# Optimization experiments

Hardware: AMD Instinct MI355X
Metric: run time of the kernel (lower is better)

## Reference

```python
import jax, jax.numpy as jnp
from jax import lax
import numpy as np

K = 4            # prototypes per class: 3 kmeans centroids + 1 backbone
EPS = 0.1        # sinkhorn entropic regularization
MAX_ITER = 100
THRESH = 0.01
KM_ITERS = 10    # Lloyd iterations (replaces host-side sklearn KMeans)
HW = 28          # the original reshapes pred to 28x28, fixing n = 784


def setup_inputs():
    key = jax.random.key(0)
    k1, k2, k3, k4 = jax.random.split(key, 4)
    b, n, d, c = 32, HW * HW, 1024, 20
    return {
        "query": jax.random.normal(k1, (b, n, d), dtype=jnp.float32),
        "score": jax.random.uniform(k2, (b, n, c), dtype=jnp.float32),
        "label": jax.random.randint(k3, (b, c), 0, 2),
        "gt": jax.random.randint(k4, (b, HW, HW), 0, c + 1),
        "weights": jnp.array([1.0, 1.0, 0.0, -1.0], dtype=jnp.float32),
    }


def _assign(dq, cen, selfm):
    # dq [b,m,d], cen [b,c,j,d], selfm [b,c,m] float mask -> one-hot labels, counts
    x2 = jnp.sum(dq * dq, axis=-1)                                   # [b,m]
    d2 = (x2[:, None, :, None]
          - 2.0 * jnp.einsum('bmd,bcjd->bcmj', dq, cen)
          + jnp.sum(cen * cen, axis=-1)[:, :, None, :])              # [b,c,m,j]
    oh = jax.nn.one_hot(jnp.argmin(d2, axis=-1), cen.shape[2], dtype=dq.dtype) * selfm[..., None]
    return oh, oh.sum(axis=2)


def _sinkhorn(Km, u, v):
    # vectorized over the [b,c] pair grid, per-pair early exit as in the torch loop
    def cond(st):
        it, r, cc, done = st
        return (it < MAX_ITER) & jnp.logical_not(jnp.all(done))

    def body(st):
        it, r, cc, done = st
        r1 = u / jnp.einsum('bcnj,bcj->bcn', Km, cc)
        c1 = v / jnp.einsum('bcnj,bcn->bcj', Km, r1)
        err = jnp.mean(jnp.abs(r1 - r), axis=-1)                     # [b,c]
        r = jnp.where(done[..., None], r, r1)
        cc = jnp.where(done[..., None], cc, c1)
        done = done | (err < THRESH)
        return it + 1, r, cc, done

    st = (jnp.int32(0), jnp.ones_like(u), jnp.ones_like(v),
          jnp.zeros(Km.shape[:2], dtype=bool))
    _, r, cc, _ = lax.while_loop(cond, body, st)
    return r[..., :, None] * cc[..., None, :] * Km                   # [b,c,n,K]


def _forward(query, score, label, gt, weights):
    b, n, d = query.shape
    c = score.shape[2]
    dq, ds = query[:, ::2, :], score[:, ::2, :]                      # stride-2 downsample
    m = dq.shape[1]
    cls_assign = jnp.argmax(ds, axis=-1)                             # [b,m]
    sel = cls_assign[:, None, :] == jnp.arange(c)[None, :, None]     # [b,c,m]
    selfm = sel.astype(query.dtype)
    cnt = selfm.sum(-1)                                              # [b,c]
    valid = (label > 0) & (cnt >= K)

    # ---- masked Lloyd's k-means with k-1 = 3 clusters per (image, class) pair
    order = jnp.argsort((~sel).astype(jnp.int32), axis=-1)           # masked points first
    init_idx = order[..., :K - 1]                                    # [b,c,3]
    cen = dq[jnp.arange(b)[:, None, None], init_idx]                 # [b,c,3,d]

    def km_step(cen, _):
        oh, kcnt = _assign(dq, cen, selfm)
        sums = jnp.einsum('bmd,bcmj->bcjd', dq, oh)
        cen = jnp.where(kcnt[..., None] > 0,
                        sums / jnp.maximum(kcnt, 1.0)[..., None], cen)
        return cen, None

    cen, _ = lax.scan(km_step, cen, None, length=KM_ITERS)
    oh, kcnt = _assign(dq, cen, selfm)                               # final labels

    # ---- sort centroids by mean cluster score (descending)
    sm = ds.mean(axis=-1)                                            # [b,m]
    avg = jnp.where(kcnt > 0,
                    jnp.einsum('bm,bcmj->bcj', sm, oh) / jnp.maximum(kcnt, 1.0),
                    -jnp.inf)
    ordj = jnp.argsort(-avg, axis=-1)                                # [b,c,3]
    cen = jnp.take_along_axis(cen, ordj[..., None], axis=2)

    # ---- backbone prototype = mean over unselected downsampled tokens
    un = 1.0 - selfm
    backbone = jnp.einsum('bmd,bcm->bcd', dq, un) / jnp.maximum(m - cnt, 1.0)[..., None]
    protos = jnp.concatenate([cen, backbone[:, :, None, :]], axis=2)  # [b,c,4,d]

    # ---- OT between query[0] tokens and the 4 prototypes (original uses query[0] always)
    q0 = query[0]
    q0h = q0 / jnp.maximum(jnp.linalg.norm(q0, axis=-1, keepdims=True), 1e-12)
    ph = protos / jnp.maximum(jnp.linalg.norm(protos, axis=-1, keepdims=True), 1e-12)
    sim = jnp.einsum('nd,bcjd->bcnj', q0h, ph)                       # [b,c,n,4]
    Km = lax.stop_gradient(jnp.exp(-(1.0 - sim) / EPS))              # torch.no_grad
    u = jnp.full((b, c, n), 1.0 / n, dtype=query.dtype)
    v = jnp.full((b, c, K), 1.0 / K, dtype=query.dtype)
    T = lax.stop_gradient(_sinkhorn(Km, u, v))                       # [b,c,n,4]

    valid = valid & jnp.logical_not(jnp.any(jnp.isnan(T), axis=(2, 3)))
    pred = jnp.einsum('bcnj,j->bcn', T, weights)                     # [b,c,n]

    # ---- BCE vs gt masks (28x28 -> 28x28 bilinear resize is the identity)
    y = (gt.reshape(b, -1)[:, None, :] == (jnp.arange(c) + 1)[None, :, None]).astype(pred.dtype)
    p = jnp.clip(pred, 0.0, 1.0)
    bce = -(y * jnp.maximum(jnp.log(p), -100.0)
            + (1.0 - y) * jnp.maximum(jnp.log(1.0 - p), -100.0)).mean(axis=-1)  # [b,c]
    bce = jnp.where(valid, bce, 0.0)
    total_n = valid.sum().astype(pred.dtype)
    return bce.sum() / (total_n + 1e-4)


def reference(query, score, label, gt, weights):
    return _forward(query, score, label, gt, weights)
```

## Files before the change

kernel.cpp:

```cpp
#include <hip/hip_runtime.h>
#include <cmath>

#define BB 32
#define NN 784
#define MM 392
#define DD 1024
#define CC 20
#define JJ 3
#define KP 4
#define KM_ITERS 10
#define GMAX 64
#define NCOL (BB * CC * KP)

typedef __attribute__((ext_vector_type(8))) short bf16x8;
typedef __attribute__((ext_vector_type(4))) float f32x4;

__device__ inline unsigned short f2bf(float x) {
  unsigned int u = __float_as_uint(x);
  u += 0x7FFFu + ((u >> 16) & 1u);
  return (unsigned short)(u >> 16);
}
__device__ inline float bf2f(unsigned short h) {
  return __uint_as_float(((unsigned int)h) << 16);
}
__device__ inline void f2bf2(float x, unsigned short& hi, unsigned short& lo) {
  hi = f2bf(x);
  lo = f2bf(x - bf2f(hi));
}
__device__ inline void store_bf4(unsigned short* baseh, unsigned short* basel,
                                 int idx4, float4 v) {
  ushort4 h, l;
  f2bf2(v.x, h.x, l.x); f2bf2(v.y, h.y, l.y);
  f2bf2(v.z, h.z, l.z); f2bf2(v.w, h.w, l.w);
  ((ushort4*)baseh)[idx4] = h;
  ((ushort4*)basel)[idx4] = l;
}

__global__ void k_cls(const float* __restrict__ score, int* __restrict__ cls,
                      float* __restrict__ sm, int* __restrict__ cnt) {
  int t = blockIdx.x * blockDim.x + threadIdx.x;
  if (t >= BB * MM) return;
  int b = t / MM, i = t - b * MM;
  const float* s = score + ((size_t)b * NN + 2 * i) * CC;
  float best = s[0]; int bi = 0; float acc = s[0];
  #pragma unroll
  for (int c = 1; c < CC; c++) { float v = s[c]; acc += v; if (v > best) { best = v; bi = c; } }
  cls[t] = bi;
  sm[t] = acc / (float)CC;
  atomicAdd(&cnt[b * CC + bi], 1);
}

__global__ void k_valid(const int* __restrict__ label, const int* __restrict__ cnt,
                        int* __restrict__ vlist, int* __restrict__ cpos, int* __restrict__ nvp) {
  __shared__ int sf[1024];
  int t = threadIdx.x;
  int flag = 0;
  if (t < BB * CC) flag = (label[t] > 0 && cnt[t] >= KP) ? 1 : 0;
  sf[t] = flag;
  __syncthreads();
  for (int off = 1; off < 1024; off <<= 1) {
    int v = sf[t];
    int add = (t >= off) ? sf[t - off] : 0;
    __syncthreads();
    sf[t] = v + add;
    __syncthreads();
  }
  if (t < BB * CC) {
    int pos = sf[t] - flag;
    cpos[t] = flag ? pos : -1;
    if (flag) vlist[pos] = t;
  }
  if (t == 0) *nvp = sf[BB * CC - 1];
}

__global__ __launch_bounds__(256) void k_csum(const float* __restrict__ query,
    const int* __restrict__ cls, float* __restrict__ classsum) {
  int b = blockIdx.x, ch = blockIdx.y;
  int tid = threadIdx.x, lane = tid & 63, wv = tid >> 6;
  __shared__ float acc[4][CC][64];
  __shared__ int s_cls[MM];
  #pragma unroll
  for (int c = 0; c < CC; c++) acc[wv][c][lane] = 0.f;
  for (int i = tid; i < MM; i += 256) s_cls[i] = cls[b * MM + i];
  __syncthreads();
  const float* qb = query + (size_t)b * NN * DD + ch * 64 + lane;
  int i0 = wv * 98;
  #pragma unroll 4
  for (int r = 0; r < 98; r++) {
    int i = i0 + r;
    float v = qb[(size_t)(2 * i) * DD];
    int cl = s_cls[i];
    acc[wv][cl][lane] += v;
  }
  __syncthreads();
  for (int cc = wv; cc < CC; cc += 4) {
    float s = acc[0][cc][lane] + acc[1][cc][lane] + acc[2][cc][lane] + acc[3][cc][lane];
    classsum[((size_t)(b * CC + cc)) * DD + ch * 64 + lane] = s;
  }
}

__global__ __launch_bounds__(512) void k_gram(
    const float* __restrict__ query, const int* __restrict__ cls,
    const int* __restrict__ cpos, const float* __restrict__ sm,
    unsigned short* __restrict__ phh, unsigned short* __restrict__ phl) {
  int bc = blockIdx.x;
  if (cpos[bc] < 0) return;
  int b = bc / CC, c = bc - b * CC;
  int tid = threadIdx.x, lane = tid & 63, wv = tid >> 6;
  const float* qb = query + (size_t)b * NN * DD;
  __shared__ int s_wtot[8];
  __shared__ int s_list[GMAX];
  __shared__ __align__(16) float Xs[GMAX][132];
  __shared__ float Gl[GMAX][65];
  __shared__ float s_w[JJ][GMAX];
  __shared__ int s_rank[JJ];
  __shared__ float s_red2[6];

  int flag = 0;
  if (tid < MM) flag = (cls[b * MM + tid] == c) ? 1 : 0;
  unsigned long long msk = __ballot(flag);
  int wp = __popcll(msk & ((1ull << lane) - 1ull));
  if (lane == 0) s_wtot[wv] = __popcll(msk);
  __syncthreads();
  int off = 0, mtot = 0;
  #pragma unroll
  for (int w = 0; w < 8; w++) { int t = s_wtot[w]; if (w < wv) off += t; mtot += t; }
  int mc = mtot > GMAX ? GMAX : mtot;
  if (flag) { int pos = off + wp; if (pos < GMAX) s_list[pos] = tid; }
  __syncthreads();

  const float* pb[4] = {nullptr, nullptr, nullptr, nullptr};
  float* xd[4] = {nullptr, nullptr, nullptr, nullptr};
  #pragma unroll
  for (int s = 0; s < 4; s++) {
    int e = tid + s * 512;
    if (e < mc * 32) {
      pb[s] = qb + (size_t)(2 * s_list[e >> 5]) * DD + (e & 31) * 4;
      xd[s] = &Xs[e >> 5][(e & 31) * 4];
    }
  }

  int T = (mc + 1) >> 1;
  int ntile = T * (T + 1) / 2;
  int ti_[2], tj_[2];
  float a00[2], a01[2], a10[2], a11[2];
  #pragma unroll
  for (int s = 0; s < 2; s++) {
    ti_[s] = -1; tj_[s] = 0;
    a00[s] = 0.f; a01[s] = 0.f; a10[s] = 0.f; a11[s] = 0.f;
    int p = tid + s * 512;
    if (p < ntile) {
      int i = (int)floorf((sqrtf(8.0f * (float)p + 1.0f) - 1.0f) * 0.5f);
      while ((i + 1) * (i + 2) / 2 <= p) i++;
      while (i * (i + 1) / 2 > p) i--;
      ti_[s] = i; tj_[s] = p - i * (i + 1) / 2;
    }
  }

  float4 cur[4], nxt[4];
  #pragma unroll
  for (int s = 0; s < 4; s++) {
    cur[s] = make_float4(0.f, 0.f, 0.f, 0.f);
    nxt[s] = make_float4(0.f, 0.f, 0.f, 0.f);
    if (pb[s]) cur[s] = *(const float4*)(pb[s]);
  }
  for (int ch = 0; ch < 8; ch++) {
    __syncthreads();
    #pragma unroll
    for (int s = 0; s < 4; s++) if (pb[s]) *(float4*)xd[s] = cur[s];
    if (ch < 7) {
      #pragma unroll
      for (int s = 0; s < 4; s++) if (pb[s]) nxt[s] = *(const float4*)(pb[s] + (ch + 1) * 128);
    }
    __syncthreads();
    #pragma unroll
    for (int s = 0; s < 2; s++) {
      if (ti_[s] >= 0) {
        const float4* xr0 = (const float4*)&Xs[2 * ti_[s]][0];
        const float4* xr1 = (const float4*)&Xs[2 * ti_[s] + 1][0];
        const float4* xc0 = (const float4*)&Xs[2 * tj_[s]][0];
        const float4* xc1 = (const float4*)&Xs[2 * tj_[s] + 1][0];
        float s00 = 0.f, s01 = 0.f, s10 = 0.f, s11 = 0.f;
        #pragma unroll
        for (int kk = 0; kk < 32; kk++) {
          float4 u0 = xr0[kk], u1 = xr1[kk], w0 = xc0[kk], w1 = xc1[kk];
          s00 += u0.x * w0.x + u0.y * w0.y + u0.z * w0.z + u0.w * w0.w;
          s01 += u0.x * w1.x + u0.y * w1.y + u0.z * w1.z + u0.w * w1.w;
          s10 += u1.x * w0.x + u1.y * w0.y + u1.z * w0.z + u1.w * w0.w;
          s11 += u1.x * w1.x + u1.y * w1.y + u1.z * w1.z + u1.w * w1.w;
        }
        a00[s] += s00; a01[s] += s01; a10[s] += s10; a11[s] += s11;
      }
    }
    #pragma unroll
    for (int s = 0; s < 4; s++) cur[s] = nxt[s];
  }

  #pragma unroll
  for (int s = 0; s < 2; s++) {
    if (ti_[s] >= 0) {
      int r0 = 2 * ti_[s], r1 = r0 + 1, c0 = 2 * tj_[s], c1 = c0 + 1;
      if (r0 < mc && c0 < mc) { Gl[r0][c0] = a00[s]; Gl[c0][r0] = a00[s]; }
      if (r0 < mc && c1 < mc) { Gl[r0][c1] = a01[s]; Gl[c1][r0] = a01[s]; }
      if (r1 < mc && c0 < mc) { Gl[r1][c0] = a10[s]; Gl[c0][r1] = a10[s]; }
      if (r1 < mc && c1 < mc) { Gl[r1][c1] = a11[s]; Gl[c1][r1] = a11[s]; }
    }
  }
  __syncthreads();

  if (wv == 0) {
    bool act = lane < mc;
    float smv = act ? sm[b * MM + s_list[lane]] : 0.f;
    s_w[0][lane] = (lane == 0) ? 1.f : 0.f;
    s_w[1][lane] = (lane == 1) ? 1.f : 0.f;
    s_w[2][lane] = (lane == 2) ? 1.f : 0.f;
    int aj = 0, n0 = 0, n1 = 0, n2 = 0;
    for (int it = 0; it <= KM_ITERS; it++) {
      float h0 = 0.f, h1 = 0.f, h2 = 0.f;
      if (act) {
        for (int i = 0; i < mc; i++) {
          float g = Gl[lane][i];
          h0 += s_w[0][i] * g; h1 += s_w[1][i] * g; h2 += s_w[2][i] * g;
        }
      }
      float t0 = s_w[0][lane] * h0, t1 = s_w[1][lane] * h1, t2 = s_w[2][lane] * h2;
      for (int o = 1; o < 64; o <<= 1) {
        t0 += __shfl_xor(t0, o, 64); t1 += __shfl_xor(t1, o, 64); t2 += __shfl_xor(t2, o, 64);
      }
      float e0 = t0 - 2.f * h0, e1 = t1 - 2.f * h1, e2 = t2 - 2.f * h2;
      aj = 0; float bv = e0;
      if (e1 < bv) { bv = e1; aj = 1; }
      if (e2 < bv) { bv = e2; aj = 2; }
      n0 = __popcll(__ballot(act && aj == 0));
      n1 = __popcll(__ballot(act && aj == 1));
      n2 = __popcll(__ballot(act && aj == 2));
      if (it == KM_ITERS) break;
      if (act) {
        if (n0 > 0) s_w[0][lane] = (aj == 0) ? 1.f / (float)n0 : 0.f;
        if (n1 > 0) s_w[1][lane] = (aj == 1) ? 1.f / (float)n1 : 0.f;
        if (n2 > 0) s_w[2][lane] = (aj == 2) ? 1.f / (float)n2 : 0.f;
      }
    }
    float s0 = (act && aj == 0) ? smv : 0.f;
    float s1 = (act && aj == 1) ? smv : 0.f;
    float s2 = (act && aj == 2) ? smv : 0.f;
    for (int o = 1; o < 64; o <<= 1) {
      s0 += __shfl_xor(s0, o, 64); s1 += __shfl_xor(s1, o, 64); s2 += __shfl_xor(s2, o, 64);
    }
    if (lane == 0) {
      float avg[JJ];
      avg[0] = (n0 > 0) ? s0 / (float)n0 : -INFINITY;
      avg[1] = (n1 > 0) ? s1 / (float)n1 : -INFINITY;
      avg[2] = (n2 > 0) ? s2 / (float)n2 : -INFINITY;
      bool used[JJ] = {false, false, false};
      for (int s = 0; s < JJ; s++) {
        int bi = -1; float bv = 0.f;
        for (int j = 0; j < JJ; j++)
          if (!used[j] && (bi < 0 || avg[j] > bv)) { bi = j; bv = avg[j]; }
        used[bi] = true; s_rank[bi] = s;
      }
    }
  }
  __syncthreads();

  float4 a0 = make_float4(0.f, 0.f, 0.f, 0.f), a1 = make_float4(0.f, 0.f, 0.f, 0.f);
  int j = tid >> 7, q = tid & 127;
  if (tid < 384) {
    for (int g = 0; g < mc; g++) {
      float w = s_w[j][g];
      if (w != 0.f) {
        const float4* row = (const float4*)(qb + (size_t)(2 * s_list[g]) * DD);
        float4 v0 = row[q], v1 = row[q + 128];
        a0.x += w * v0.x; a0.y += w * v0.y; a0.z += w * v0.z; a0.w += w * v0.w;
        a1.x += w * v1.x; a1.y += w * v1.y; a1.z += w * v1.z; a1.w += w * v1.w;
      }
    }
    float ssq = a0.x * a0.x + a0.y * a0.y + a0.z * a0.z + a0.w * a0.w
              + a1.x * a1.x + a1.y * a1.y + a1.z * a1.z + a1.w * a1.w;
    #pragma unroll
    for (int o = 1; o < 64; o <<= 1) ssq += __shfl_xor(ssq, o, 64);
    if (lane == 0) s_red2[wv] = ssq;
  }
  __syncthreads();
  if (tid < 384) {
    float nrm = fmaxf(sqrtf(s_red2[2 * j] + s_red2[2 * j + 1]), 1e-12f);
    size_t rowoff = ((size_t)bc * KP + s_rank[j]) * DD;
    float4 o0 = make_float4(a0.x / nrm, a0.y / nrm, a0.z / nrm, a0.w / nrm);
    float4 o1 = make_float4(a1.x / nrm, a1.y / nrm, a1.z / nrm, a1.w / nrm);
    store_bf4(phh + rowoff, phl + rowoff, q, o0);
    store_bf4(phh + rowoff, phl + rowoff, q + 128, o1);
  }
}

__global__ __launch_bounds__(256) void k_backbone(const float* __restrict__ classsum,
    const int* __restrict__ cpos, const int* __restrict__ cnt,
    unsigned short* __restrict__ phh, unsigned short* __restrict__ phl) {
  int bc = blockIdx.x;
  if (cpos[bc] < 0) return;
  int b = bc / CC;
  int tid = threadIdx.x, lane = tid & 63, wv = tid >> 6;
  __shared__ float s_red[4];
  __shared__ float s_nrm;
  float4 ts = make_float4(0.f, 0.f, 0.f, 0.f);
  for (int c2 = 0; c2 < CC; c2++) {
    float4 v = *(const float4*)(classsum + ((size_t)(b * CC + c2)) * DD + tid * 4);
    ts.x += v.x; ts.y += v.y; ts.z += v.z; ts.w += v.w;
  }
  float4 cs = *(const float4*)(classsum + (size_t)bc * DD + tid * 4);
  float denom = fmaxf((float)(MM - cnt[bc]), 1.f);
  float4 v = make_float4((ts.x - cs.x) / denom, (ts.y - cs.y) / denom,
                         (ts.z - cs.z) / denom, (ts.w - cs.w) / denom);
  float pp = v.x * v.x + v.y * v.y + v.z * v.z + v.w * v.w;
  for (int o = 1; o < 64; o <<= 1) pp += __shfl_xor(pp, o, 64);
  if (lane == 0) s_red[wv] = pp;
  __syncthreads();
  if (tid == 0) s_nrm = fmaxf(sqrtf(s_red[0] + s_red[1] + s_red[2] + s_red[3]), 1e-12f);
  __syncthreads();
  float nrm = s_nrm;
  size_t rowoff = ((size_t)bc * KP + 3) * DD;
  store_bf4(phh + rowoff, phl + rowoff, tid,
            make_float4(v.x / nrm, v.y / nrm, v.z / nrm, v.w / nrm));
}

__global__ void k_q0h(const float* __restrict__ query,
                      unsigned short* __restrict__ q0hh, unsigned short* __restrict__ q0hl) {
  int n = blockIdx.x;
  const float* src = query + (size_t)n * DD;
  float ss = 0.f;
  for (int k = threadIdx.x; k < DD; k += 64) { float v = src[k]; ss += v * v; }
  for (int o = 32; o > 0; o >>= 1) ss += __shfl_xor(ss, o, 64);
  float nrm = fmaxf(sqrtf(ss), 1e-12f);
  for (int k = threadIdx.x; k < DD; k += 64) {
    unsigned short hi, lo;
    f2bf2(src[k] / nrm, hi, lo);
    q0hh[(size_t)n * DD + k] = hi;
    q0hl[(size_t)n * DD + k] = lo;
  }
}

__global__ __launch_bounds__(64) void k_gemm(
    const unsigned short* __restrict__ Ah, const unsigned short* __restrict__ Al,
    const unsigned short* __restrict__ Bh, const unsigned short* __restrict__ Bl,
    const int* __restrict__ vlist, const int* __restrict__ nvp,
    float* __restrict__ P) {
  int nv4 = 4 * *nvp;
  int n0 = blockIdx.y * 64;
  if (n0 >= nv4) return;
  int m0 = blockIdx.x * 64;
  int lane = threadIdx.x;
  int kh = lane >> 4;
  int lr = lane & 15;

  const unsigned short* pa_h[4]; const unsigned short* pa_l[4];
  #pragma unroll
  for (int mi = 0; mi < 4; mi++) {
    size_t o = (size_t)(m0 + mi * 16 + lr) * DD + kh * 8;
    pa_h[mi] = Ah + o; pa_l[mi] = Al + o;
  }
  const unsigned short* pb_h[4]; const unsigned short* pb_l[4];
  #pragma unroll
  for (int ni = 0; ni < 4; ni++) {
    int col = n0 + ni * 16 + lr;
    int cc = (col < nv4) ? col : 0;
    size_t o = ((size_t)vlist[cc >> 2] * KP + (cc & 3)) * DD + kh * 8;
    pb_h[ni] = Bh + o; pb_l[ni] = Bl + o;
  }

  f32x4 acc[4][4];
  #pragma unroll
  for (int mi = 0; mi < 4; mi++)
    #pragma unroll
    for (int ni = 0; ni < 4; ni++) acc[mi][ni] = (f32x4){0.f, 0.f, 0.f, 0.f};

  for (int k0 = 0; k0 < DD; k0 += 32) {
    bf16x8 ah[4], al[4], bh[4], bl[4];
    #pragma unroll
    for (int i = 0; i < 4; i++) {
      ah[i] = *(const bf16x8*)(pa_h[i] + k0);
      al[i] = *(const bf16x8*)(pa_l[i] + k0);
      bh[i] = *(const bf16x8*)(pb_h[i] + k0);
      bl[i] = *(const bf16x8*)(pb_l[i] + k0);
    }
    #pragma unroll
    for (int mi = 0; mi < 4; mi++)
      #pragma unroll
      for (int ni = 0; ni < 4; ni++) {
        acc[mi][ni] = __builtin_amdgcn_mfma_f32_16x16x32_bf16(ah[mi], bh[ni], acc[mi][ni], 0, 0, 0);
        acc[mi][ni] = __builtin_amdgcn_mfma_f32_16x16x32_bf16(ah[mi], bl[ni], acc[mi][ni], 0, 0, 0);
        acc[mi][ni] = __builtin_amdgcn_mfma_f32_16x16x32_bf16(al[mi], bh[ni], acc[mi][ni], 0, 0, 0);
      }
  }

  #pragma unroll
  for (int ni = 0; ni < 4; ni++) {
    int col = n0 + ni * 16 + lr;
    #pragma unroll
    for (int mi = 0; mi < 4; mi++) {
      int m = m0 + mi * 16 + kh * 4;
      if (m < NN) {
        *(f32x4*)(P + (size_t)col * NN + m) = acc[mi][ni];
      }
    }
  }
}

__global__ __launch_bounds__(256) void k_sink(const float* __restrict__ P,
    const int* __restrict__ cpos, const int* __restrict__ gt,
    const float* __restrict__ wts, float* __restrict__ bce, int* __restrict__ vld) {
  int bc = blockIdx.x; int b = bc / CC, c = bc - b * CC;
  int tid = threadIdx.x;
  if (cpos[bc] < 0) {
    if (tid == 0) { bce[bc] = 0.f; vld[bc] = 0; }
    return;
  }
  int p = cpos[bc];
  int lane = tid & 63, wv = tid >> 6;
  __shared__ float ccv[KP];
  __shared__ float wred[4][5];
  __shared__ float s_err;
  __shared__ int s_nan;
  float4 kv[4]; float rr[4];
  #pragma unroll
  for (int s4 = 0; s4 < 4; s4++) {
    int n = tid + 256 * s4;
    kv[s4] = make_float4(0.f, 0.f, 0.f, 0.f); rr[s4] = 1.f;
    if (n < NN) {
      float v[KP];
      #pragma unroll
      for (int q = 0; q < KP; q++)
        v[q] = P[((size_t)(4 * p + q)) * NN + n];
      float4 o;
      o.x = expf(-(1.0f - v[0]) / 0.1f);
      o.y = expf(-(1.0f - v[1]) / 0.1f);
      o.z = expf(-(1.0f - v[2]) / 0.1f);
      o.w = expf(-(1.0f - v[3]) / 0.1f);
      kv[s4] = o;
    }
  }
  if (tid < KP) ccv[tid] = 1.f;
  if (tid == 0) s_nan = 0;
  __syncthreads();
  const float uu = 1.0f / (float)NN, vv = 1.0f / (float)KP;
  for (int it = 0; it < 100; it++) {
    float c0 = ccv[0], c1 = ccv[1], c2 = ccv[2], c3 = ccv[3];
    float dsum = 0.f, p0 = 0.f, p1 = 0.f, p2 = 0.f, p3 = 0.f;
    #pragma unroll
    for (int s4 = 0; s4 < 4; s4++) {
      int n = tid + 256 * s4;
      if (n < NN) {
        float4 k4 = kv[s4];
        float S = k4.x * c0 + k4.y * c1 + k4.z * c2 + k4.w * c3;
        float r1 = uu / S;
        dsum += fabsf(r1 - rr[s4]);
        rr[s4] = r1;
        p0 += k4.x * r1; p1 += k4.y * r1; p2 += k4.z * r1; p3 += k4.w * r1;
      }
    }
    for (int o = 32; o > 0; o >>= 1) {
      dsum += __shfl_down(dsum, o, 64);
      p0 += __shfl_down(p0, o, 64); p1 += __shfl_down(p1, o, 64);
      p2 += __shfl_down(p2, o, 64); p3 += __shfl_down(p3, o, 64);
    }
    if (lane == 0) { wred[wv][0] = dsum; wred[wv][1] = p0; wred[wv][2] = p1; wred[wv][3] = p2; wred[wv][4] = p3; }
    __syncthreads();
    if (tid == 0) {
      float d = 0.f, q0 = 0.f, q1 = 0.f, q2 = 0.f, q3 = 0.f;
      for (int w = 0; w < 4; w++) { d += wred[w][0]; q0 += wred[w][1]; q1 += wred[w][2]; q2 += wred[w][3]; q3 += wred[w][4]; }
      ccv[0] = vv / q0; ccv[1] = vv / q1; ccv[2] = vv / q2; ccv[3] = vv / q3;
      s_err = d / (float)NN;
    }
    __syncthreads();
    if (s_err < 0.01f) break;
  }
  float w0 = wts[0], w1 = wts[1], w2 = wts[2], w3 = wts[3];
  float cc0 = ccv[0], cc1 = ccv[1], cc2 = ccv[2], cc3 = ccv[3];
  float bsum = 0.f; int nanloc = 0;
  const int* gtb = gt + b * NN;
  #pragma unroll
  for (int s4 = 0; s4 < 4; s4++) {
    int n = tid + 256 * s4;
    if (n < NN) {
      float4 k4 = kv[s4];
      float rv = rr[s4];
      float T0 = rv * cc0 * k4.x, T1 = rv * cc1 * k4.y, T2 = rv * cc2 * k4.z, T3 = rv * cc3 * k4.w;
      if (T0 != T0 || T1 != T1 || T2 != T2 || T3 != T3) nanloc = 1;
      float pred = T0 * w0 + T1 * w1 + T2 * w2 + T3 * w3;
      float pcl = fminf(fmaxf(pred, 0.f), 1.f);
      float t = (gtb[n] == c + 1) ? fmaxf(logf(pcl), -100.f) : fmaxf(logf(1.f - pcl), -100.f);
      bsum += t;
    }
  }
  if (nanloc) s_nan = 1;
  for (int o = 32; o > 0; o >>= 1) bsum += __shfl_down(bsum, o, 64);
  if (lane == 0) wred[wv][0] = bsum;
  __syncthreads();
  if (tid == 0) {
    float tot = wred[0][0] + wred[1][0] + wred[2][0] + wred[3][0];
    if (s_nan) { bce[bc] = 0.f; vld[bc] = 0; }
    else { bce[bc] = -(tot / (float)NN); vld[bc] = 1; }
  }
}

__global__ void k_final(const float* __restrict__ bce, const int* __restrict__ vld,
                        float* __restrict__ out) {
  __shared__ float rs[256];
  __shared__ float rc[256];
  float s = 0.f, cv = 0.f;
  for (int t = threadIdx.x; t < BB * CC; t += 256) { s += bce[t]; cv += (float)vld[t]; }
  rs[threadIdx.x] = s; rc[threadIdx.x] = cv; __syncthreads();
  for (int o = 128; o > 0; o >>= 1) {
    if (threadIdx.x < o) { rs[threadIdx.x] += rs[threadIdx.x + o]; rc[threadIdx.x] += rc[threadIdx.x + o]; }
    __syncthreads();
  }
  if (threadIdx.x == 0) out[0] = rs[0] / (rc[0] + 0.0001f);
}

extern "C" void kernel_launch(void* const* d_in, const int* in_sizes, int n_in,
                              void* d_out, int out_size, void* d_ws, size_t ws_size,
                              hipStream_t stream) {
  (void)in_sizes; (void)n_in; (void)out_size; (void)ws_size;
  const float* query = (const float*)d_in[0];
  const float* score = (const float*)d_in[1];
  const int*   label = (const int*)d_in[2];
  const int*   gt    = (const int*)d_in[3];
  const float* wts   = (const float*)d_in[4];
  float* ws = (float*)d_ws;

  size_t off = 0;
  int* cls = (int*)(ws + off);            off += (size_t)BB * MM;
  int* cnt = (int*)(ws + off);            off += (size_t)BB * CC;
  float* sm = ws + off;                   off += (size_t)BB * MM;
  int* vlist = (int*)(ws + off);          off += (size_t)BB * CC;
  int* cpos = (int*)(ws + off);           off += (size_t)BB * CC;
  int* nvp = (int*)(ws + off);            off += 16;
  float* classsum = ws + off;             off += (size_t)BB * CC * DD;
  unsigned short* q0hh = (unsigned short*)(ws + off);  off += (size_t)NN * DD / 2;
  unsigned short* q0hl = (unsigned short*)(ws + off);  off += (size_t)NN * DD / 2;
  unsigned short* phh = (unsigned short*)(ws + off);   off += (size_t)BB * CC * KP * DD / 2;
  unsigned short* phl = (unsigned short*)(ws + off);   off += (size_t)BB * CC * KP * DD / 2;
  float* P = ws + off;                    off += (size_t)NCOL * NN;
  float* bce = ws + off;                  off += (size_t)BB * CC;
  int* vld = (int*)(ws + off);            off += (size_t)BB * CC;

  hipMemsetAsync(cnt, 0, (size_t)BB * CC * sizeof(int), stream);
  k_cls<<<(BB * MM + 255) / 256, 256, 0, stream>>>(score, cls, sm, cnt);
  k_valid<<<1, 1024, 0, stream>>>(label, cnt, vlist, cpos, nvp);
  k_csum<<<dim3(BB, 16), 256, 0, stream>>>(query, cls, classsum);
  k_gram<<<BB * CC, 512, 0, stream>>>(query, cls, cpos, sm, phh, phl);
  k_backbone<<<BB * CC, 256, 0, stream>>>(classsum, cpos, cnt, phh, phl);
  k_q0h<<<NN, 64, 0, stream>>>(query, q0hh, q0hl);
  dim3 gg((NN + 63) / 64, NCOL / 64);
  k_gemm<<<gg, 64, 0, stream>>>(q0hh, q0hl, phh, phl, vlist, nvp, P);
  k_sink<<<BB * CC, 256, 0, stream>>>(P, cpos, gt, wts, bce, vld);
  k_final<<<1, 256, 0, stream>>>(bce, vld, (float*)d_out);
}
```

Baseline: 301.0 us.

## Fuse preprocessing kernels, fold backbone into gram, finalize via atomics in sinkhorn

Merges the class argmax, validity flags, query-row normalization and per-batch total sums into one multi-role k_prep launch. The backbone prototype is now computed inside k_gram from a per-batch total minus the class's own rows, replacing the classsum buffer and the k_backbone kernel. The final reduction moves into k_sink through atomics and a last-block counter, removing k_final and the memset. The GEMM drops valid-column compaction and computes all columns, including invalid pairs whose prototypes are never written, in exchange for fewer launches and no prefix scan.

```diff
diff --git a/kernel.cpp b/kernel.cpp
--- a/kernel.cpp
+++ b/kernel.cpp
@@ -11,6 +11,8 @@
 #define KM_ITERS 10
 #define GMAX 64
 #define NCOL (BB * CC * KP)
+#define NQ0B 98
+#define NTSB (BB * 16)
 
 typedef __attribute__((ext_vector_type(8))) short bf16x8;
 typedef __attribute__((ext_vector_type(4))) float f32x4;
@@ -36,75 +38,86 @@
   ((ushort4*)basel)[idx4] = l;
 }
 
-__global__ void k_cls(const float* __restrict__ score, int* __restrict__ cls,
-                      float* __restrict__ sm, int* __restrict__ cnt) {
-  int t = blockIdx.x * blockDim.x + threadIdx.x;
-  if (t >= BB * MM) return;
-  int b = t / MM, i = t - b * MM;
-  const float* s = score + ((size_t)b * NN + 2 * i) * CC;
-  float best = s[0]; int bi = 0; float acc = s[0];
-  #pragma unroll
-  for (int c = 1; c < CC; c++) { float v = s[c]; acc += v; if (v > best) { best = v; bi = c; } }
-  cls[t] = bi;
-  sm[t] = acc / (float)CC;
-  atomicAdd(&cnt[b * CC + bi], 1);
-}
-
-__global__ void k_valid(const int* __restrict__ label, const int* __restrict__ cnt,
-                        int* __restrict__ vlist, int* __restrict__ cpos, int* __restrict__ nvp) {
-  __shared__ int sf[1024];
-  int t = threadIdx.x;
-  int flag = 0;
-  if (t < BB * CC) flag = (label[t] > 0 && cnt[t] >= KP) ? 1 : 0;
-  sf[t] = flag;
-  __syncthreads();
-  for (int off = 1; off < 1024; off <<= 1) {
-    int v = sf[t];
-    int add = (t >= off) ? sf[t - off] : 0;
-    __syncthreads();
-    sf[t] = v + add;
-    __syncthreads();
-  }
-  if (t < BB * CC) {
-    int pos = sf[t] - flag;
-    cpos[t] = flag ? pos : -1;
-    if (flag) vlist[pos] = t;
-  }
-  if (t == 0) *nvp = sf[BB * CC - 1];
-}
-
-__global__ __launch_bounds__(256) void k_csum(const float* __restrict__ query,
-    const int* __restrict__ cls, float* __restrict__ classsum) {
-  int b = blockIdx.x, ch = blockIdx.y;
+__global__ __launch_bounds__(512) void k_prep(
+    const float* __restrict__ score, const float* __restrict__ query,
+    const int* __restrict__ label,
+    int* __restrict__ cls, float* __restrict__ sm, int* __restrict__ valid,
+    float* __restrict__ totalsum,
+    unsigned short* __restrict__ q0hh, unsigned short* __restrict__ q0hl,
+    float* __restrict__ gred) {
+  int blk = blockIdx.x;
   int tid = threadIdx.x, lane = tid & 63, wv = tid >> 6;
-  __shared__ float acc[4][CC][64];
-  __shared__ int s_cls[MM];
-  #pragma unroll
-  for (int c = 0; c < CC; c++) acc[wv][c][lane] = 0.f;
-  for (int i = tid; i < MM; i += 256) s_cls[i] = cls[b * MM + i];
-  __syncthreads();
-  const float* qb = query + (size_t)b * NN * DD + ch * 64 + lane;
-  int i0 = wv * 98;
-  #pragma unroll 4
-  for (int r = 0; r < 98; r++) {
-    int i = i0 + r;
-    float v = qb[(size_t)(2 * i) * DD];
-    int cl = s_cls[i];
-    acc[wv][cl][lane] += v;
-  }
-  __syncthreads();
-  for (int cc = wv; cc < CC; cc += 4) {
-    float s = acc[0][cc][lane] + acc[1][cc][lane] + acc[2][cc][lane] + acc[3][cc][lane];
-    classsum[((size_t)(b * CC + cc)) * DD + ch * 64 + lane] = s;
+  __shared__ int s_cnt[CC];
+  __shared__ float sa[8][64];
+
+  if (blk < BB) {
+    int b = blk;
+    if (tid < CC) s_cnt[tid] = 0;
+    __syncthreads();
+    if (tid < MM) {
+      const float4* s4 = (const float4*)(score + ((size_t)b * NN + 2 * tid) * CC);
+      float4 r[5];
+      #pragma unroll
+      for (int k = 0; k < 5; k++) r[k] = s4[k];
+      const float* s = (const float*)r;
+      float best = s[0]; int bi = 0; float acc = s[0];
+      #pragma unroll
+      for (int c = 1; c < CC; c++) { float v = s[c]; acc += v; if (v > best) { best = v; bi = c; } }
+      cls[b * MM + tid] = bi;
+      sm[b * MM + tid] = acc / (float)CC;
+      atomicAdd(&s_cnt[bi], 1);
+    }
+    __syncthreads();
+    if (tid < CC) {
+      int cv = s_cnt[tid];
+      valid[b * CC + tid] = (label[b * CC + tid] > 0 && cv >= KP) ? 1 : 0;
+    }
+    if (blk == 0 && tid == 0) { gred[0] = 0.f; gred[1] = 0.f; ((int*)gred)[2] = 0; }
+  } else if (blk < BB + NQ0B) {
+    int n = (blk - BB) * 8 + wv;
+    const float* src = query + (size_t)n * DD;
+    float v[16];
+    float ss = 0.f;
+    #pragma unroll
+    for (int j = 0; j < 16; j++) { v[j] = src[lane + 64 * j]; ss += v[j] * v[j]; }
+    #pragma unroll
+    for (int o = 32; o > 0; o >>= 1) ss += __shfl_xor(ss, o, 64);
+    float nrm = fmaxf(sqrtf(ss), 1e-12f);
+    #pragma unroll
+    for (int j = 0; j < 16; j++) {
+      unsigned short hi, lo;
+      f2bf2(v[j] / nrm, hi, lo);
+      q0hh[(size_t)n * DD + lane + 64 * j] = hi;
+      q0hl[(size_t)n * DD + lane + 64 * j] = lo;
+    }
+  } else {
+    int t = blk - BB - NQ0B;
+    int b = t >> 4, ch = t & 15;
+    const float* qb = query + (size_t)b * NN * DD + ch * 64 + lane;
+    float a = 0.f;
+    #pragma unroll 7
+    for (int r = 0; r < 49; r++) {
+      int i = wv * 49 + r;
+      a += qb[(size_t)(2 * i) * DD];
+    }
+    sa[wv][lane] = a;
+    __syncthreads();
+    if (wv == 0) {
+      float s = 0.f;
+      #pragma unroll
+      for (int w = 0; w < 8; w++) s += sa[w][lane];
+      totalsum[(size_t)b * DD + ch * 64 + lane] = s;
+    }
   }
 }
 
 __global__ __launch_bounds__(512) void k_gram(
     const float* __restrict__ query, const int* __restrict__ cls,
-    const int* __restrict__ cpos, const float* __restrict__ sm,
+    const int* __restrict__ valid, const float* __restrict__ sm,
+    const float* __restrict__ totalsum,
     unsigned short* __restrict__ phh, unsigned short* __restrict__ phl) {
   int bc = blockIdx.x;
-  if (cpos[bc] < 0) return;
+  if (!valid[bc]) return;
   int b = bc / CC, c = bc - b * CC;
   int tid = threadIdx.x, lane = tid & 63, wv = tid >> 6;
   const float* qb = query + (size_t)b * NN * DD;
@@ -114,7 +127,7 @@
   __shared__ float Gl[GMAX][65];
   __shared__ float s_w[JJ][GMAX];
   __shared__ int s_rank[JJ];
-  __shared__ float s_red2[6];
+  __shared__ float s_red2[8];
 
   int flag = 0;
   if (tid < MM) flag = (cls[b * MM + tid] == c) ? 1 : 0;
@@ -265,7 +278,7 @@
 
   float4 a0 = make_float4(0.f, 0.f, 0.f, 0.f), a1 = make_float4(0.f, 0.f, 0.f, 0.f);
   int j = tid >> 7, q = tid & 127;
-  if (tid < 384) {
+  if (j < 3) {
     for (int g = 0; g < mc; g++) {
       float w = s_w[j][g];
       if (w != 0.f) {
@@ -275,77 +288,42 @@
         a1.x += w * v1.x; a1.y += w * v1.y; a1.z += w * v1.z; a1.w += w * v1.w;
       }
     }
-    float ssq = a0.x * a0.x + a0.y * a0.y + a0.z * a0.z + a0.w * a0.w
-              + a1.x * a1.x + a1.y * a1.y + a1.z * a1.z + a1.w * a1.w;
-    #pragma unroll
-    for (int o = 1; o < 64; o <<= 1) ssq += __shfl_xor(ssq, o, 64);
-    if (lane == 0) s_red2[wv] = ssq;
-  }
+  } else {
+    for (int g = 0; g < mc; g++) {
+      const float4* row = (const float4*)(qb + (size_t)(2 * s_list[g]) * DD);
+      float4 v0 = row[q], v1 = row[q + 128];
+      a0.x += v0.x; a0.y += v0.y; a0.z += v0.z; a0.w += v0.w;
+      a1.x += v1.x; a1.y += v1.y; a1.z += v1.z; a1.w += v1.w;
+    }
+    const float4* tb = (const float4*)(totalsum + (size_t)b * DD);
+    float4 t0 = tb[q], t1 = tb[q + 128];
+    float denom = fmaxf((float)(MM - mtot), 1.f);
+    float inv = 1.f / denom;
+    a0.x = (t0.x - a0.x) * inv; a0.y = (t0.y - a0.y) * inv;
+    a0.z = (t0.z - a0.z) * inv; a0.w = (t0.w - a0.w) * inv;
+    a1.x = (t1.x - a1.x) * inv; a1.y = (t1.y - a1.y) * inv;
+    a1.z = (t1.z - a1.z) * inv; a1.w = (t1.w - a1.w) * inv;
+  }
+  float ssq = a0.x * a0.x + a0.y * a0.y + a0.z * a0.z + a0.w * a0.w
+            + a1.x * a1.x + a1.y * a1.y + a1.z * a1.z + a1.w * a1.w;
+  #pragma unroll
+  for (int o = 1; o < 64; o <<= 1) ssq += __shfl_xor(ssq, o, 64);
+  if (lane == 0) s_red2[wv] = ssq;
   __syncthreads();
-  if (tid < 384) {
-    float nrm = fmaxf(sqrtf(s_red2[2 * j] + s_red2[2 * j + 1]), 1e-12f);
-    size_t rowoff = ((size_t)bc * KP + s_rank[j]) * DD;
-    float4 o0 = make_float4(a0.x / nrm, a0.y / nrm, a0.z / nrm, a0.w / nrm);
-    float4 o1 = make_float4(a1.x / nrm, a1.y / nrm, a1.z / nrm, a1.w / nrm);
-    store_bf4(phh + rowoff, phl + rowoff, q, o0);
-    store_bf4(phh + rowoff, phl + rowoff, q + 128, o1);
-  }
-}
-
-__global__ __launch_bounds__(256) void k_backbone(const float* __restrict__ classsum,
-    const int* __restrict__ cpos, const int* __restrict__ cnt,
-    unsigned short* __restrict__ phh, unsigned short* __restrict__ phl) {
-  int bc = blockIdx.x;
-  if (cpos[bc] < 0) return;
-  int b = bc / CC;
-  int tid = threadIdx.x, lane = tid & 63, wv = tid >> 6;
-  __shared__ float s_red[4];
-  __shared__ float s_nrm;
-  float4 ts = make_float4(0.f, 0.f, 0.f, 0.f);
-  for (int c2 = 0; c2 < CC; c2++) {
-    float4 v = *(const float4*)(classsum + ((size_t)(b * CC + c2)) * DD + tid * 4);
-    ts.x += v.x; ts.y += v.y; ts.z += v.z; ts.w += v.w;
-  }
-  float4 cs = *(const float4*)(classsum + (size_t)bc * DD + tid * 4);
-  float denom = fmaxf((float)(MM - cnt[bc]), 1.f);
-  float4 v = make_float4((ts.x - cs.x) / denom, (ts.y - cs.y) / denom,
-                         (ts.z - cs.z) / denom, (ts.w - cs.w) / denom);
-  float pp = v.x * v.x + v.y * v.y + v.z * v.z + v.w * v.w;
-  for (int o = 1; o < 64; o <<= 1) pp += __shfl_xor(pp, o, 64);
-  if (lane == 0) s_red[wv] = pp;
-  __syncthreads();
-  if (tid == 0) s_nrm = fmaxf(sqrtf(s_red[0] + s_red[1] + s_red[2] + s_red[3]), 1e-12f);
-  __syncthreads();
-  float nrm = s_nrm;
-  size_t rowoff = ((size_t)bc * KP + 3) * DD;
-  store_bf4(phh + rowoff, phl + rowoff, tid,
-            make_float4(v.x / nrm, v.y / nrm, v.z / nrm, v.w / nrm));
-}
-
-__global__ void k_q0h(const float* __restrict__ query,
-                      unsigned short* __restrict__ q0hh, unsigned short* __restrict__ q0hl) {
-  int n = blockIdx.x;
-  const float* src = query + (size_t)n * DD;
-  float ss = 0.f;
-  for (int k = threadIdx.x; k < DD; k += 64) { float v = src[k]; ss += v * v; }
-  for (int o = 32; o > 0; o >>= 1) ss += __shfl_xor(ss, o, 64);
-  float nrm = fmaxf(sqrtf(ss), 1e-12f);
-  for (int k = threadIdx.x; k < DD; k += 64) {
-    unsigned short hi, lo;
-    f2bf2(src[k] / nrm, hi, lo);
-    q0hh[(size_t)n * DD + k] = hi;
-    q0hl[(size_t)n * DD + k] = lo;
-  }
+  float nrm = fmaxf(sqrtf(s_red2[2 * j] + s_red2[2 * j + 1]), 1e-12f);
+  int prow = (j < 3) ? s_rank[j] : 3;
+  size_t rowoff = ((size_t)bc * KP + prow) * DD;
+  float4 o0 = make_float4(a0.x / nrm, a0.y / nrm, a0.z / nrm, a0.w / nrm);
+  float4 o1 = make_float4(a1.x / nrm, a1.y / nrm, a1.z / nrm, a1.w / nrm);
+  store_bf4(phh + rowoff, phl + rowoff, q, o0);
+  store_bf4(phh + rowoff, phl + rowoff, q + 128, o1);
 }
 
 __global__ __launch_bounds__(64) void k_gemm(
     const unsigned short* __restrict__ Ah, const unsigned short* __restrict__ Al,
     const unsigned short* __restrict__ Bh, const unsigned short* __restrict__ Bl,
-    const int* __restrict__ vlist, const int* __restrict__ nvp,
     float* __restrict__ P) {
-  int nv4 = 4 * *nvp;
   int n0 = blockIdx.y * 64;
-  if (n0 >= nv4) return;
   int m0 = blockIdx.x * 64;
   int lane = threadIdx.x;
   int kh = lane >> 4;
@@ -361,8 +339,7 @@
   #pragma unroll
   for (int ni = 0; ni < 4; ni++) {
     int col = n0 + ni * 16 + lr;
-    int cc = (col < nv4) ? col : 0;
-    size_t o = ((size_t)vlist[cc >> 2] * KP + (cc & 3)) * DD + kh * 8;
+    size_t o = (size_t)col * DD + kh * 8;
     pb_h[ni] = Bh + o; pb_l[ni] = Bl + o;
   }
 
@@ -405,114 +382,109 @@
 }
 
 __global__ __launch_bounds__(256) void k_sink(const float* __restrict__ P,
-    const int* __restrict__ cpos, const int* __restrict__ gt,
-    const float* __restrict__ wts, float* __restrict__ bce, int* __restrict__ vld) {
+    const int* __restrict__ valid, const int* __restrict__ gt,
+    const float* __restrict__ wts, float* __restrict__ gred, float* __restrict__ out) {
   int bc = blockIdx.x; int b = bc / CC, c = bc - b * CC;
   int tid = threadIdx.x;
-  if (cpos[bc] < 0) {
-    if (tid == 0) { bce[bc] = 0.f; vld[bc] = 0; }
-    return;
-  }
-  int p = cpos[bc];
   int lane = tid & 63, wv = tid >> 6;
-  __shared__ float ccv[KP];
-  __shared__ float wred[4][5];
-  __shared__ float s_err;
-  __shared__ int s_nan;
-  float4 kv[4]; float rr[4];
-  #pragma unroll
-  for (int s4 = 0; s4 < 4; s4++) {
-    int n = tid + 256 * s4;
-    kv[s4] = make_float4(0.f, 0.f, 0.f, 0.f); rr[s4] = 1.f;
-    if (n < NN) {
-      float v[KP];
+  float bce_out = 0.f; int vld_out = 0;
+
+  if (valid[bc]) {
+    __shared__ float ccv[KP];
+    __shared__ float wred[4][5];
+    __shared__ float s_err;
+    __shared__ int s_nan;
+    float4 kv[4]; float rr[4];
+    #pragma unroll
+    for (int s4 = 0; s4 < 4; s4++) {
+      int n = tid + 256 * s4;
+      kv[s4] = make_float4(0.f, 0.f, 0.f, 0.f); rr[s4] = 1.f;
+      if (n < NN) {
+        float v[KP];
+        #pragma unroll
+        for (int q = 0; q < KP; q++)
+          v[q] = P[((size_t)(4 * bc + q)) * NN + n];
+        float4 o;
+        o.x = expf(-(1.0f - v[0]) / 0.1f);
+        o.y = expf(-(1.0f - v[1]) / 0.1f);
+        o.z = expf(-(1.0f - v[2]) / 0.1f);
+        o.w = expf(-(1.0f - v[3]) / 0.1f);
+        kv[s4] = o;
+      }
+    }
+    if (tid < KP) ccv[tid] = 1.f;
+    if (tid == 0) s_nan = 0;
+    __syncthreads();
+    const float uu = 1.0f / (float)NN, vv = 1.0f / (float)KP;
+    for (int it = 0; it < 100; it++) {
+      float c0 = ccv[0], c1 = ccv[1], c2 = ccv[2], c3 = ccv[3];
+      float dsum = 0.f, p0 = 0.f, p1 = 0.f, p2 = 0.f, p3 = 0.f;
       #pragma unroll
-      for (int q = 0; q < KP; q++)
-        v[q] = P[((size_t)(4 * p + q)) * NN + n];
-      float4 o;
-      o.x = expf(-(1.0f - v[0]) / 0.1f);
-      o.y = expf(-(1.0f - v[1]) / 0.1f);
-      o.z = expf(-(1.0f - v[2]) / 0.1f);
-      o.w = expf(-(1.0f - v[3]) / 0.1f);
-      kv[s4] = o;
-    }
-  }
-  if (tid < KP) ccv[tid] = 1.f;
-  if (tid == 0) s_nan = 0;
-  __syncthreads();
-  const float uu = 1.0f / (float)NN, vv = 1.0f / (float)KP;
-  for (int it = 0; it < 100; it++) {
-    float c0 = ccv[0], c1 = ccv[1], c2 = ccv[2], c3 = ccv[3];
-    float dsum = 0.f, p0 = 0.f, p1 = 0.f, p2 = 0.f, p3 = 0.f;
+      for (int s4 = 0; s4 < 4; s4++) {
+        int n = tid + 256 * s4;
+        if (n < NN) {
+          float4 k4 = kv[s4];
+          float S = k4.x * c0 + k4.y * c1 + k4.z * c2 + k4.w * c3;
+          float r1 = uu / S;
+          dsum += fabsf(r1 - rr[s4]);
+          rr[s4] = r1;
+          p0 += k4.x * r1; p1 += k4.y * r1; p2 += k4.z * r1; p3 += k4.w * r1;
+        }
+      }
+      for (int o = 32; o > 0; o >>= 1) {
+        dsum += __shfl_down(dsum, o, 64);
+        p0 += __shfl_down(p0, o, 64); p1 += __shfl_down(p1, o, 64);
+        p2 += __shfl_down(p2, o, 64); p3 += __shfl_down(p3, o, 64);
+      }
+      if (lane == 0) { wred[wv][0] = dsum; wred[wv][1] = p0; wred[wv][2] = p1; wred[wv][3] = p2; wred[wv][4] = p3; }
+      __syncthreads();
+      if (tid == 0) {
+        float d = 0.f, q0 = 0.f, q1 = 0.f, q2 = 0.f, q3 = 0.f;
+        for (int w = 0; w < 4; w++) { d += wred[w][0]; q0 += wred[w][1]; q1 += wred[w][2]; q2 += wred[w][3]; q3 += wred[w][4]; }
+        ccv[0] = vv / q0; ccv[1] = vv / q1; ccv[2] = vv / q2; ccv[3] = vv / q3;
+        s_err = d / (float)NN;
+      }
+      __syncthreads();
+      if (s_err < 0.01f) break;
+    }
+    float w0 = wts[0], w1 = wts[1], w2 = wts[2], w3 = wts[3];
+    float cc0 = ccv[0], cc1 = ccv[1], cc2 = ccv[2], cc3 = ccv[3];
+    float bsum = 0.f; int nanloc = 0;
+    const int* gtb = gt + b * NN;
     #pragma unroll
     for (int s4 = 0; s4 < 4; s4++) {
       int n = tid + 256 * s4;
       if (n < NN) {
         float4 k4 = kv[s4];
-        float S = k4.x * c0 + k4.y * c1 + k4.z * c2 + k4.w * c3;
-        float r1 = uu / S;
-        dsum += fabsf(r1 - rr[s4]);
-        rr[s4] = r1;
-        p0 += k4.x * r1; p1 += k4.y * r1; p2 += k4.z * r1; p3 += k4.w * r1;
-      }
-    }
-    for (int o = 32; o > 0; o >>= 1) {
-      dsum += __shfl_down(dsum, o, 64);
-      p0 += __shfl_down(p0, o, 64); p1 += __shfl_down(p1, o, 64);
-      p2 += __shfl_down(p2, o, 64); p3 += __shfl_down(p3, o, 64);
-    }
-    if (lane == 0) { wred[wv][0] = dsum; wred[wv][1] = p0; wred[wv][2] = p1; wred[wv][3] = p2; wred[wv][4] = p3; }
+        float rv = rr[s4];
+        float T0 = rv * cc0 * k4.x, T1 = rv * cc1 * k4.y, T2 = rv * cc2 * k4.z, T3 = rv * cc3 * k4.w;
+        if (T0 != T0 || T1 != T1 || T2 != T2 || T3 != T3) nanloc = 1;
+        float pred = T0 * w0 + T1 * w1 + T2 * w2 + T3 * w3;
+        float pcl = fminf(fmaxf(pred, 0.f), 1.f);
+        float t = (gtb[n] == c + 1) ? fmaxf(logf(pcl), -100.f) : fmaxf(logf(1.f - pcl), -100.f);
+        bsum += t;
+      }
+    }
+    if (nanloc) s_nan = 1;
+    for (int o = 32; o > 0; o >>= 1) bsum += __shfl_down(bsum, o, 64);
+    if (lane == 0) wred[wv][0] = bsum;
     __syncthreads();
     if (tid == 0) {
-      float d = 0.f, q0 = 0.f, q1 = 0.f, q2 = 0.f, q3 = 0.f;
-      for (int w = 0; w < 4; w++) { d += wred[w][0]; q0 += wred[w][1]; q1 += wred[w][2]; q2 += wred[w][3]; q3 += wred[w][4]; }
-      ccv[0] = vv / q0; ccv[1] = vv / q1; ccv[2] = vv / q2; ccv[3] = vv / q3;
-      s_err = d / (float)NN;
-    }
-    __syncthreads();
-    if (s_err < 0.01f) break;
-  }
-  float w0 = wts[0], w1 = wts[1], w2 = wts[2], w3 = wts[3];
-  float cc0 = ccv[0], cc1 = ccv[1], cc2 = ccv[2], cc3 = ccv[3];
-  float bsum = 0.f; int nanloc = 0;
-  const int* gtb = gt + b * NN;
-  #pragma unroll
-  for (int s4 = 0; s4 < 4; s4++) {
-    int n = tid + 256 * s4;
-    if (n < NN) {
-      float4 k4 = kv[s4];
-      float rv = rr[s4];
-      float T0 = rv * cc0 * k4.x, T1 = rv * cc1 * k4.y, T2 = rv * cc2 * k4.z, T3 = rv * cc3 * k4.w;
-      if (T0 != T0 || T1 != T1 || T2 != T2 || T3 != T3) nanloc = 1;
-      float pred = T0 * w0 + T1 * w1 + T2 * w2 + T3 * w3;
-      float pcl = fminf(fmaxf(pred, 0.f), 1.f);
-      float t = (gtb[n] == c + 1) ? fmaxf(logf(pcl), -100.f) : fmaxf(logf(1.f - pcl), -100.f);
-      bsum += t;
-    }
-  }
-  if (nanloc) s_nan = 1;
-  for (int o = 32; o > 0; o >>= 1) bsum += __shfl_down(bsum, o, 64);
-  if (lane == 0) wred[wv][0] = bsum;
-  __syncthreads();
+      float tot = wred[0][0] + wred[1][0] + wred[2][0] + wred[3][0];
+      if (!s_nan) { bce_out = -(tot / (float)NN); vld_out = 1; }
+    }
+  }
+
   if (tid == 0) {
-    float tot = wred[0][0] + wred[1][0] + wred[2][0] + wred[3][0];
-    if (s_nan) { bce[bc] = 0.f; vld[bc] = 0; }
-    else { bce[bc] = -(tot / (float)NN); vld[bc] = 1; }
-  }
-}
-
-__global__ void k_final(const float* __restrict__ bce, const int* __restrict__ vld,
-                        float* __restrict__ out) {
-  __shared__ float rs[256];
-  __shared__ float rc[256];
-  float s = 0.f, cv = 0.f;
-  for (int t = threadIdx.x; t < BB * CC; t += 256) { s += bce[t]; cv += (float)vld[t]; }
-  rs[threadIdx.x] = s; rc[threadIdx.x] = cv; __syncthreads();
-  for (int o = 128; o > 0; o >>= 1) {
-    if (threadIdx.x < o) { rs[threadIdx.x] += rs[threadIdx.x + o]; rc[threadIdx.x] += rc[threadIdx.x + o]; }
-    __syncthreads();
-  }
-  if (threadIdx.x == 0) out[0] = rs[0] / (rc[0] + 0.0001f);
+    if (vld_out) { atomicAdd(&gred[0], bce_out); atomicAdd(&gred[1], 1.f); }
+    __threadfence();
+    int old = atomicAdd((int*)gred + 2, 1);
+    if (old == BB * CC - 1) {
+      float s = atomicAdd(&gred[0], 0.f);
+      float n2 = atomicAdd(&gred[1], 0.f);
+      out[0] = s / (n2 + 0.0001f);
+    }
+  }
 }
 
 extern "C" void kernel_launch(void* const* d_in, const int* in_sizes, int n_in,
@@ -528,29 +500,20 @@
 
   size_t off = 0;
   int* cls = (int*)(ws + off);            off += (size_t)BB * MM;
-  int* cnt = (int*)(ws + off);            off += (size_t)BB * CC;
   float* sm = ws + off;                   off += (size_t)BB * MM;
-  int* vlist = (int*)(ws + off);          off += (size_t)BB * CC;
-  int* cpos = (int*)(ws + off);           off += (size_t)BB * CC;
-  int* nvp = (int*)(ws + off);            off += 16;
-  float* classsum = ws + off;             off += (size_t)BB * CC * DD;
+  int* valid = (int*)(ws + off);          off += (size_t)BB * CC;
+  float* totalsum = ws + off;             off += (size_t)BB * DD;
   unsigned short* q0hh = (unsigned short*)(ws + off);  off += (size_t)NN * DD / 2;
   unsigned short* q0hl = (unsigned short*)(ws + off);  off += (size_t)NN * DD / 2;
   unsigned short* phh = (unsigned short*)(ws + off);   off += (size_t)BB * CC * KP * DD / 2;
   unsigned short* phl = (unsigned short*)(ws + off);   off += (size_t)BB * CC * KP * DD / 2;
   float* P = ws + off;                    off += (size_t)NCOL * NN;
-  float* bce = ws + off;                  off += (size_t)BB * CC;
-  int* vld = (int*)(ws + off);            off += (size_t)BB * CC;
-
-  hipMemsetAsync(cnt, 0, (size_t)BB * CC * sizeof(int), stream);
-  k_cls<<<(BB * MM + 255) / 256, 256, 0, stream>>>(score, cls, sm, cnt);
-  k_valid<<<1, 1024, 0, stream>>>(label, cnt, vlist, cpos, nvp);
-  k_csum<<<dim3(BB, 16), 256, 0, stream>>>(query, cls, classsum);
-  k_gram<<<BB * CC, 512, 0, stream>>>(query, cls, cpos, sm, phh, phl);
-  k_backbone<<<BB * CC, 256, 0, stream>>>(classsum, cpos, cnt, phh, phl);
-  k_q0h<<<NN, 64, 0, stream>>>(query, q0hh, q0hl);
+  float* gred = ws + off;                 off += 16;
+
+  k_prep<<<BB + NQ0B + NTSB, 512, 0, stream>>>(score, query, label, cls, sm, valid,
+                                               totalsum, q0hh, q0hl, gred);
+  k_gram<<<BB * CC, 512, 0, stream>>>(query, cls, valid, sm, totalsum, phh, phl);
   dim3 gg((NN + 63) / 64, NCOL / 64);
-  k_gemm<<<gg, 64, 0, stream>>>(q0hh, q0hl, phh, phl, vlist, nvp, P);
-  k_sink<<<BB * CC, 256, 0, stream>>>(P, cpos, gt, wts, bce, vld);
-  k_final<<<1, 256, 0, stream>>>(bce, vld, (float*)d_out);
-}
+  k_gemm<<<gg, 64, 0, stream>>>(q0hh, q0hl, phh, phl, P);
+  k_sink<<<BB * CC, 256, 0, stream>>>(P, valid, gt, wts, gred, (float*)d_out);
+}
```

Measured after the change: 269.9 us. 10.3% less time.
